# Performance work log

Hardware: AMD Instinct MI355X
Metric: run time of the kernel (lower is better)

Reference implementation:

```python
import jax, jax.numpy as jnp
import numpy as np

B, T = 32, 256
CHAR_V, BICHAR_V, CTYPE_V = 10000, 200000, 8
CD, BD, TD = 100, 100, 20
LIN, H = 200, 200
IN_DIMS = 2 * CD + 2 * BD + TD  # 420


def lstm_scan(xs, Wih, Whh, b, reverse=False):
    # xs: [T, B, LIN]; Wih: [4H, LIN]; Whh: [4H, H]; b: [4H]
    h0 = jnp.zeros((xs.shape[1], Whh.shape[1]), xs.dtype)
    c0 = jnp.zeros_like(h0)

    def step(carry, x):
        h, c = carry
        g = x @ Wih.T + h @ Whh.T + b  # [B, 4H]
        i, f, gg, o = jnp.split(g, 4, axis=-1)  # torch LSTMCell gate order
        c = jax.nn.sigmoid(f) * c + jax.nn.sigmoid(i) * jnp.tanh(gg)
        h = jax.nn.sigmoid(o) * jnp.tanh(c)
        return (h, c), h

    _, hs = jax.lax.scan(step, (h0, c0), xs, reverse=reverse)
    return hs  # [T, B, H]


def setup_inputs() -> dict:
    key = jax.random.key(0)
    ks = jax.random.split(key, 20)
    d = {
        "chars": jax.random.randint(ks[0], (B, T), 0, CHAR_V, jnp.int32),
        "left_bichar": jax.random.randint(ks[1], (B, T), 0, BICHAR_V, jnp.int32),
        "right_bichar": jax.random.randint(ks[2], (B, T), 0, BICHAR_V, jnp.int32),
        "extchars": jax.random.randint(ks[3], (B, T), 0, CHAR_V, jnp.int32),
        "extleft_bichar": jax.random.randint(ks[4], (B, T), 0, BICHAR_V, jnp.int32),
        "extright_bichar": jax.random.randint(ks[5], (B, T), 0, BICHAR_V, jnp.int32),
        "char_type": jax.random.randint(ks[6], (B, T), 0, CTYPE_V, jnp.int32),
        "E_char": jax.random.normal(ks[7], (CHAR_V, CD), jnp.float32) * 0.1,
        "E_extchar": jax.random.normal(ks[8], (CHAR_V, CD), jnp.float32) * 0.1,
        "E_bichar": jax.random.normal(ks[9], (BICHAR_V, BD), jnp.float32) * 0.1,
        "E_extbichar": jax.random.normal(ks[10], (BICHAR_V, BD), jnp.float32) * 0.1,
        "E_ctype": jax.random.normal(ks[11], (CTYPE_V, TD), jnp.float32) * 0.1,
        "fc_w": jax.random.normal(ks[12], (LIN, IN_DIMS), jnp.float32) * (1.0 / np.sqrt(IN_DIMS)),
        "fc_b": jnp.zeros((LIN,), jnp.float32),
        "Wih_l": jax.random.normal(ks[13], (4 * H, LIN), jnp.float32) * (1.0 / np.sqrt(LIN)),
        "Whh_l": jax.random.normal(ks[14], (4 * H, H), jnp.float32) * (1.0 / np.sqrt(H)),
        "b_l": jnp.zeros((4 * H,), jnp.float32),
        "Wih_r": jax.random.normal(ks[15], (4 * H, LIN), jnp.float32) * (1.0 / np.sqrt(LIN)),
        "Whh_r": jax.random.normal(ks[16], (4 * H, H), jnp.float32) * (1.0 / np.sqrt(H)),
        "b_r": jnp.zeros((4 * H,), jnp.float32),
    }
    return d


def reference(chars, left_bichar, right_bichar, extchars, extleft_bichar,
              extright_bichar, char_type, E_char, E_extchar, E_bichar,
              E_extbichar, E_ctype, fc_w, fc_b, Wih_l, Whh_l, b_l,
              Wih_r, Whh_r, b_r):
    c_e = E_char[chars]            # [B,T,CD]
    ec_e = E_extchar[extchars]
    lb_e = E_bichar[left_bichar]   # [B,T,BD]
    elb_e = E_extbichar[extleft_bichar]
    rb_e = E_bichar[right_bichar]
    erb_e = E_extbichar[extright_bichar]
    ct_e = E_ctype[char_type]      # [B,T,TD]

    left_total = jnp.concatenate([c_e, ec_e, lb_e, elb_e, ct_e], axis=2)
    right_total = jnp.concatenate([c_e, ec_e, rb_e, erb_e, ct_e], axis=2)

    left_x = jnp.tanh(left_total @ fc_w.T + fc_b).transpose(1, 0, 2)   # [T,B,LIN]
    right_x = jnp.tanh(right_total @ fc_w.T + fc_b).transpose(1, 0, 2)

    left_hs = lstm_scan(left_x, Wih_l, Whh_l, b_l, reverse=False)   # [T,B,H]
    right_hs = lstm_scan(right_x, Wih_r, Whh_r, b_r, reverse=True)  # [T,B,H]

    out = jnp.concatenate([left_hs, right_hs], axis=2).transpose(1, 0, 2)  # [B,T,2H]
    return out
```

## Files before the change

kernel.cpp:

```cpp
#include <hip/hip_runtime.h>
#include <stdint.h>

#define B_    32
#define T_    256
#define CD    100
#define BD    100
#define TD    20
#define LIN   200
#define HD    200
#define INDIM 420
#define G4    800

typedef __attribute__((ext_vector_type(8))) short bfrag8;
typedef __attribute__((ext_vector_type(4))) float f32x4v;

static __device__ __forceinline__ unsigned short f2bf(float f) {
  unsigned u = __float_as_uint(f);
  u = u + 0x7fffu + ((u >> 16) & 1u);
  return (unsigned short)(u >> 16);
}
static __device__ __forceinline__ float bf2f(unsigned short s) {
  return __uint_as_float(((unsigned)s) << 16);
}
static __device__ __forceinline__ float sigm(float x) {
  return __builtin_amdgcn_rcpf(1.0f + __builtin_amdgcn_exp2f(x * -1.4426950408889634f));
}
static __device__ __forceinline__ float tanhx(float x) {
  return 1.0f - 2.0f * __builtin_amdgcn_rcpf(1.0f + __builtin_amdgcn_exp2f(x * 2.8853900817779268f));
}

static __device__ __forceinline__ void mk_hilo(float4 a, float4 b, bfrag8& hi, bfrag8& lo) {
  float q[8] = {a.x, a.y, a.z, a.w, b.x, b.y, b.z, b.w};
  #pragma unroll
  for (int j = 0; j < 8; ++j) {
    unsigned short h = f2bf(q[j]);
    hi[j] = (short)h;
    lo[j] = (short)f2bf(q[j] - bf2f(h));
  }
}
static __device__ __forceinline__ bfrag8 mk_hi(float4 a, float4 b) {
  bfrag8 r;
  float q[8] = {a.x, a.y, a.z, a.w, b.x, b.y, b.z, b.w};
  #pragma unroll
  for (int j = 0; j < 8; ++j) r[j] = (short)f2bf(q[j]);
  return r;
}

__global__ void presplit_kernel(const float* __restrict__ fc_w,
                                const float* __restrict__ Wih_l,
                                const float* __restrict__ Wih_r,
                                unsigned short* __restrict__ fcw_hi,
                                unsigned short* __restrict__ fcw_lo,
                                unsigned short* __restrict__ wih_hi,
                                unsigned short* __restrict__ wih_lo) {
  int tid = blockIdx.x * blockDim.x + threadIdx.x;
  int stride = gridDim.x * blockDim.x;
  for (int i = tid; i < 13 * 14 * 512; i += stride) {
    int j = i & 7, l = (i >> 3) & 63, f = i >> 9;
    int kt = f % 14, nt = f / 14;
    int n = nt * 16 + (l & 15);
    int k = kt * 32 + ((l >> 4) << 3) + j;
    float v = (n < LIN && k < INDIM) ? fc_w[n * INDIM + k] : 0.0f;
    unsigned short h = f2bf(v);
    fcw_hi[i] = h;
    fcw_lo[i] = f2bf(v - bf2f(h));
  }
  for (int d = 0; d < 2; ++d) {
    const float* W = d ? Wih_r : Wih_l;
    unsigned short* oh = wih_hi + (size_t)d * 179200;
    unsigned short* ol = wih_lo + (size_t)d * 179200;
    for (int i = tid; i < 50 * 7 * 512; i += stride) {
      int j = i & 7, l = (i >> 3) & 63, f = i >> 9;
      int kt = f % 7, nt = f / 7;
      int np = nt * 16 + (l & 15);
      int no = (np & 3) * 200 + (np >> 2);
      int k = kt * 32 + ((l >> 4) << 3) + j;
      float v = (k < LIN) ? W[no * LIN + k] : 0.0f;
      unsigned short h = f2bf(v);
      oh[i] = h;
      ol[i] = f2bf(v - bf2f(h));
    }
  }
}

__global__ __launch_bounds__(256) void fc_kernel(
    const int* __restrict__ chars, const int* __restrict__ left_bichar,
    const int* __restrict__ right_bichar, const int* __restrict__ extchars,
    const int* __restrict__ extleft, const int* __restrict__ extright,
    const int* __restrict__ ctype,
    const float* __restrict__ E_char, const float* __restrict__ E_extchar,
    const float* __restrict__ E_bichar, const float* __restrict__ E_extbichar,
    const float* __restrict__ E_ctype, const float* __restrict__ fc_b,
    const unsigned short* __restrict__ fcw_hi, const unsigned short* __restrict__ fcw_lo,
    float* __restrict__ x) {
  __shared__ __align__(16) float feat[32 * 452];
  int rb = blockIdx.x;
  int dir = rb >> 8;
  int t = rb & 255;
  int tid = threadIdx.x;
  const int* bi  = dir ? right_bichar : left_bichar;
  const int* ebi = dir ? extright : extleft;

  for (int cc = tid; cc < 32 * 113; cc += 256) {
    int lr = cc / 113, kc = cc - lr * 113;
    int k = kc << 2;
    float4 v = make_float4(0.f, 0.f, 0.f, 0.f);
    if (k < INDIM) {
      int id; const float* tab; int kk; int wdt;
      if (k < 100)      { id = chars[lr * T_ + t];    tab = E_char;      kk = k;       wdt = 100; }
      else if (k < 200) { id = extchars[lr * T_ + t]; tab = E_extchar;   kk = k - 100; wdt = 100; }
      else if (k < 300) { id = bi[lr * T_ + t];       tab = E_bichar;    kk = k - 200; wdt = 100; }
      else if (k < 400) { id = ebi[lr * T_ + t];      tab = E_extbichar; kk = k - 300; wdt = 100; }
      else              { id = ctype[lr * T_ + t];    tab = E_ctype;     kk = k - 400; wdt = 20;  }
      v = *reinterpret_cast<const float4*>(tab + (size_t)id * wdt + kk);
    }
    *reinterpret_cast<float4*>(&feat[lr * 452 + k]) = v;
  }
  __syncthreads();

  int w = tid >> 6, l = tid & 63;
  int lrow = l & 15, lk8 = (l >> 4) << 3;
  f32x4v acc[8];
  #pragma unroll
  for (int i = 0; i < 8; ++i) acc[i] = (f32x4v){0.f, 0.f, 0.f, 0.f};

  for (int kt = 0; kt < 14; ++kt) {
    bfrag8 ah[2], al[2];
    #pragma unroll
    for (int mt = 0; mt < 2; ++mt) {
      const float* fp = &feat[(mt * 16 + lrow) * 452 + kt * 32 + lk8];
      float4 v0 = *reinterpret_cast<const float4*>(fp);
      float4 v1 = *reinterpret_cast<const float4*>(fp + 4);
      mk_hilo(v0, v1, ah[mt], al[mt]);
    }
    #pragma unroll
    for (int s = 0; s < 4; ++s) {
      int nt = w + (s << 2);
      if (nt < 13) {
        size_t fo = ((size_t)(nt * 14 + kt) * 64 + l) * 8;
        bfrag8 bh = *reinterpret_cast<const bfrag8*>(fcw_hi + fo);
        bfrag8 bl = *reinterpret_cast<const bfrag8*>(fcw_lo + fo);
        #pragma unroll
        for (int mt = 0; mt < 2; ++mt) {
          acc[s * 2 + mt] = __builtin_amdgcn_mfma_f32_16x16x32_bf16(ah[mt], bh, acc[s * 2 + mt], 0, 0, 0);
          acc[s * 2 + mt] = __builtin_amdgcn_mfma_f32_16x16x32_bf16(al[mt], bh, acc[s * 2 + mt], 0, 0, 0);
          acc[s * 2 + mt] = __builtin_amdgcn_mfma_f32_16x16x32_bf16(ah[mt], bl, acc[s * 2 + mt], 0, 0, 0);
        }
      }
    }
  }
  int r0 = rb * 32;
  #pragma unroll
  for (int s = 0; s < 4; ++s) {
    int nt = w + (s << 2);
    if (nt < 13) {
      int n = nt * 16 + lrow;
      if (n < LIN) {
        float bias = fc_b[n];
        #pragma unroll
        for (int mt = 0; mt < 2; ++mt) {
          #pragma unroll
          for (int rr = 0; rr < 4; ++rr) {
            int row = mt * 16 + ((l >> 4) << 2) + rr;
            x[(size_t)(r0 + row) * LIN + n] = tanhx(acc[s * 2 + mt][rr] + bias);
          }
        }
      }
    }
  }
}

__global__ __launch_bounds__(512) void xwih_kernel(
    const float* __restrict__ x, const unsigned short* __restrict__ wih_hi,
    const unsigned short* __restrict__ wih_lo, const float* __restrict__ b_l,
    const float* __restrict__ b_r, float* __restrict__ pre) {
  int bid = blockIdx.x;
  int dir = (bid >= 320) ? 1 : 0;
  int rem = bid - dir * 320;
  int rbm = rem / 5, nb = rem - rbm * 5;
  int m0 = rbm * 128, n0 = nb * 160;
  int tid = threadIdx.x, w = tid >> 6, l = tid & 63;
  int lrow = l & 15, lk8 = (l >> 4) << 3;
  const float* xd = x + (size_t)dir * 8192 * LIN;
  const unsigned short* wh = wih_hi + (size_t)dir * 179200;
  const unsigned short* wl = wih_lo + (size_t)dir * 179200;
  const float* bias = dir ? b_r : b_l;

  f32x4v acc[10];
  #pragma unroll
  for (int i = 0; i < 10; ++i) acc[i] = (f32x4v){0.f, 0.f, 0.f, 0.f};

  int row = m0 + w * 16 + lrow;
  for (int kt = 0; kt < 7; ++kt) {
    int kb = kt * 32 + lk8;
    bfrag8 ah = {0,0,0,0,0,0,0,0}, al = {0,0,0,0,0,0,0,0};
    if (kb <= 192) {
      const float* fp = xd + (size_t)row * LIN + kb;
      float4 v0 = *reinterpret_cast<const float4*>(fp);
      float4 v1 = *reinterpret_cast<const float4*>(fp + 4);
      mk_hilo(v0, v1, ah, al);
    }
    #pragma unroll
    for (int nt = 0; nt < 10; ++nt) {
      int ntg = nb * 10 + nt;
      size_t fo = ((size_t)(ntg * 7 + kt) * 64 + l) * 8;
      bfrag8 bh = *reinterpret_cast<const bfrag8*>(wh + fo);
      bfrag8 bl = *reinterpret_cast<const bfrag8*>(wl + fo);
      acc[nt] = __builtin_amdgcn_mfma_f32_16x16x32_bf16(ah, bh, acc[nt], 0, 0, 0);
      acc[nt] = __builtin_amdgcn_mfma_f32_16x16x32_bf16(al, bh, acc[nt], 0, 0, 0);
      acc[nt] = __builtin_amdgcn_mfma_f32_16x16x32_bf16(ah, bl, acc[nt], 0, 0, 0);
    }
  }
  #pragma unroll
  for (int nt = 0; nt < 10; ++nt) {
    int n = n0 + nt * 16 + lrow;
    float bb = bias[(n & 3) * 200 + (n >> 2)];
    int hcol = n >> 2, g = n & 3;
    int i6 = hcol >> 5;
    int hc5 = hcol & 31;
    int wv = hc5 >> 2, lhi = hc5 & 3;
    int chunk = (i6 < 6) ? (i6 * 8 + wv) : (48 + wv);
    #pragma unroll
    for (int rr = 0; rr < 4; ++rr) {
      int r2 = m0 + w * 16 + ((l >> 4) << 2) + rr;
      int t = r2 >> 5, b32 = r2 & 31;
      int hf2 = b32 >> 4, b = b32 & 15;
      int lane = b + 16 * lhi;
      size_t dst = ((((size_t)(dir * 2 + hf2) * 256 + t) * 50 + chunk) * 64 + lane) * 4 + g;
      pre[dst] = acc[nt][rr] + bb;
    }
  }
}

__global__ __launch_bounds__(512, 2) void lstm_kernel(
    const float* __restrict__ pre, const float* __restrict__ Whh_l,
    const float* __restrict__ Whh_r, float* __restrict__ out) {
  __shared__ __align__(16) unsigned short hbufA[3584];
  __shared__ __align__(16) unsigned short hbufB[3584];
  __shared__ __align__(16) unsigned short whx[35840];

  int bi = blockIdx.x;
  int dir = bi >> 1, half = bi & 1;
  const float* Whh = dir ? Whh_r : Whh_l;
  int tid = threadIdx.x, w = tid >> 6, l = tid & 63;
  int lrow = l & 15, lk8 = (l >> 4) << 3;

  bfrag8 Breg[5][7];
  #pragma unroll
  for (int i = 0; i < 5; ++i) {
    int np = (w + 8 * i) * 16 + lrow;
    int no = (np & 3) * 200 + (np >> 2);
    #pragma unroll
    for (int kt = 0; kt < 7; ++kt) {
      int kb = kt * 32 + lk8;
      bfrag8 bb = {0,0,0,0,0,0,0,0};
      if (kb <= 192) {
        const float* fp = Whh + (size_t)no * HD + kb;
        bb = mk_hi(*reinterpret_cast<const float4*>(fp),
                   *reinterpret_cast<const float4*>(fp + 4));
      }
      Breg[i][kt] = bb;
    }
  }
  for (int e = tid; e < 4480; e += 512) {
    int l2 = e & 63, f = e >> 6;
    int kt = f % 7, tile = f / 7;
    int np = (40 + tile) * 16 + (l2 & 15);
    int no = (np & 3) * 200 + (np >> 2);
    int kb = kt * 32 + ((l2 >> 4) << 3);
    bfrag8 bb = {0,0,0,0,0,0,0,0};
    if (kb <= 192) {
      const float* fp = Whh + (size_t)no * HD + kb;
      bb = mk_hi(*reinterpret_cast<const float4*>(fp),
                 *reinterpret_cast<const float4*>(fp + 4));
    }
    *reinterpret_cast<bfrag8*>(&whx[(size_t)e * 8]) = bb;
  }
  for (int e = tid; e < 896; e += 512) {
    reinterpret_cast<uint64_t*>(hbufA)[e] = 0;
    reinterpret_cast<uint64_t*>(hbufB)[e] = 0;
  }
  float c[7];
  #pragma unroll
  for (int i = 0; i < 7; ++i) c[i] = 0.f;

  int hbase = 4 * w + (l >> 4);
  int hw = (lrow + 16 * ((hbase >> 3) & 3)) * 8 + (hbase & 7);

  const float* psrcL = pre + ((size_t)(dir * 2 + half) * 256 + (dir ? 255 : 0)) * 12800
                     + w * 256 + (l << 2);
  const int pstep = dir ? -12800 : 12800;
  float* outp = out + (size_t)((half * 16 + lrow) * 256 + (dir ? 255 : 0)) * 400
              + dir * 200 + (l >> 4) + 4 * w;
  const int ostep = dir ? -400 : 400;

  __syncthreads();

  float4 pA[7], pB[7];
  #pragma unroll
  for (int i = 0; i < 6; ++i) pA[i] = *reinterpret_cast<const float4*>(psrcL + i * 2048);
  if (w < 2) pA[6] = *reinterpret_cast<const float4*>(psrcL + 12288);
  psrcL += pstep;

  auto STEP = [&](const unsigned short* rbuf, unsigned short* wbuf,
                  float4 (&pc)[7], float4 (&pn)[7]) {
    #pragma unroll
    for (int i = 0; i < 6; ++i) pn[i] = *reinterpret_cast<const float4*>(psrcL + i * 2048);
    if (w < 2) pn[6] = *reinterpret_cast<const float4*>(psrcL + 12288);
    psrcL += pstep;
    f32x4v acc[7];
    #pragma unroll
    for (int i = 0; i < 7; ++i) acc[i] = (f32x4v){0.f, 0.f, 0.f, 0.f};
    #pragma unroll
    for (int kt = 0; kt < 7; ++kt) {
      bfrag8 hf = *reinterpret_cast<const bfrag8*>(&rbuf[kt * 512 + l * 8]);
      #pragma unroll
      for (int i = 0; i < 5; ++i)
        acc[i] = __builtin_amdgcn_mfma_f32_16x16x32_bf16(Breg[i][kt], hf, acc[i], 0, 0, 0);
      bfrag8 b5 = *reinterpret_cast<const bfrag8*>(&whx[(w * 7 + kt) * 512 + l * 8]);
      acc[5] = __builtin_amdgcn_mfma_f32_16x16x32_bf16(b5, hf, acc[5], 0, 0, 0);
      if (w < 2) {
        bfrag8 b6 = *reinterpret_cast<const bfrag8*>(&whx[((8 + w) * 7 + kt) * 512 + l * 8]);
        acc[6] = __builtin_amdgcn_mfma_f32_16x16x32_bf16(b6, hf, acc[6], 0, 0, 0);
      }
    }
    #pragma unroll
    for (int i = 0; i < 7; ++i) {
      if (i < 6 || w < 2) {
        float ig = acc[i][0] + pc[i].x;
        float fg = acc[i][1] + pc[i].y;
        float gg = acc[i][2] + pc[i].z;
        float og = acc[i][3] + pc[i].w;
        float cv = sigm(fg) * c[i] + sigm(ig) * tanhx(gg);
        c[i] = cv;
        float h = sigm(og) * tanhx(cv);
        outp[32 * i] = h;
        wbuf[hw + i * 512] = f2bf(h);
      }
    }
    outp += ostep;
    __builtin_amdgcn_sched_barrier(0x1 | 0x2 | 0x4 | 0x8);
    asm volatile("s_waitcnt lgkmcnt(0)");
    __builtin_amdgcn_s_barrier();
    __builtin_amdgcn_sched_barrier(0x1 | 0x2 | 0x4 | 0x8);
  };

  for (int it = 0; it < 128; ++it) {
    STEP(hbufA, hbufB, pA, pB);
    STEP(hbufB, hbufA, pB, pA);
  }
}

extern "C" void kernel_launch(void* const* d_in, const int* in_sizes, int n_in,
                              void* d_out, int out_size, void* d_ws, size_t ws_size,
                              hipStream_t stream) {
  (void)in_sizes; (void)n_in; (void)out_size; (void)ws_size;
  const int* chars        = (const int*)d_in[0];
  const int* left_bichar  = (const int*)d_in[1];
  const int* right_bichar = (const int*)d_in[2];
  const int* extchars     = (const int*)d_in[3];
  const int* extleft      = (const int*)d_in[4];
  const int* extright     = (const int*)d_in[5];
  const int* ctype        = (const int*)d_in[6];
  const float* E_char      = (const float*)d_in[7];
  const float* E_extchar   = (const float*)d_in[8];
  const float* E_bichar    = (const float*)d_in[9];
  const float* E_extbichar = (const float*)d_in[10];
  const float* E_ctype     = (const float*)d_in[11];
  const float* fc_w  = (const float*)d_in[12];
  const float* fc_b  = (const float*)d_in[13];
  const float* Wih_l = (const float*)d_in[14];
  const float* Whh_l = (const float*)d_in[15];
  const float* b_l   = (const float*)d_in[16];
  const float* Wih_r = (const float*)d_in[17];
  const float* Whh_r = (const float*)d_in[18];
  const float* b_r   = (const float*)d_in[19];
  float* out = (float*)d_out;
  char* ws = (char*)d_ws;

  float* x   = (float*)(ws);
  float* pre = (float*)(ws + 13107200);
  unsigned short* fcw_hi = (unsigned short*)(ws + 65536000);
  unsigned short* fcw_lo = (unsigned short*)(ws + 65722368);
  unsigned short* wih_hi = (unsigned short*)(ws + 65908736);
  unsigned short* wih_lo = (unsigned short*)(ws + 66625536);

  presplit_kernel<<<256, 256, 0, stream>>>(fc_w, Wih_l, Wih_r, fcw_hi, fcw_lo, wih_hi, wih_lo);
  fc_kernel<<<512, 256, 0, stream>>>(chars, left_bichar, right_bichar, extchars,
                                     extleft, extright, ctype, E_char, E_extchar,
                                     E_bichar, E_extbichar, E_ctype, fc_b,
                                     fcw_hi, fcw_lo, x);
  xwih_kernel<<<640, 512, 0, stream>>>(x, wih_hi, wih_lo, b_l, b_r, pre);
  lstm_kernel<<<4, 512, 0, stream>>>(pre, Whh_l, Whh_r, out);
}
```

Before: 761.5 us.

## Keep more Whh tiles in registers, seed MFMA accumulators, fuse gate reciprocals

Moves one more 16-row Whh tile per wave from LDS into registers (Breg 5→6), so only waves 0-1 read the extra tile from LDS and the per-step LDS traffic for B fragments shrinks. The precomputed input gates now initialize the MFMA accumulators instead of being added afterwards. The gate nonlinearities are algebraically combined so the cell update needs one reciprocal instead of several, with exponent arguments clamped to avoid overflow. This raises register pressure under launch_bounds(512,2), which may cause spills, and it changes rounding slightly.

Result: faster. 738.4 us (-3.0%).

```diff
diff --git a/kernel.cpp b/kernel.cpp
--- a/kernel.cpp
+++ b/kernel.cpp
@@ -27,6 +27,9 @@
 }
 static __device__ __forceinline__ float tanhx(float x) {
   return 1.0f - 2.0f * __builtin_amdgcn_rcpf(1.0f + __builtin_amdgcn_exp2f(x * 2.8853900817779268f));
+}
+static __device__ __forceinline__ float clamp40(float x) {
+  return fminf(fmaxf(x, -40.0f), 40.0f);
 }
 
 static __device__ __forceinline__ void mk_hilo(float4 a, float4 b, bfrag8& hi, bfrag8& lo) {
@@ -237,7 +240,7 @@
     const float* __restrict__ Whh_r, float* __restrict__ out) {
   __shared__ __align__(16) unsigned short hbufA[3584];
   __shared__ __align__(16) unsigned short hbufB[3584];
-  __shared__ __align__(16) unsigned short whx[35840];
+  __shared__ __align__(16) unsigned short whx[7168];
 
   int bi = blockIdx.x;
   int dir = bi >> 1, half = bi & 1;
@@ -245,9 +248,9 @@
   int tid = threadIdx.x, w = tid >> 6, l = tid & 63;
   int lrow = l & 15, lk8 = (l >> 4) << 3;
 
-  bfrag8 Breg[5][7];
-  #pragma unroll
-  for (int i = 0; i < 5; ++i) {
+  bfrag8 Breg[6][7];
+  #pragma unroll
+  for (int i = 0; i < 6; ++i) {
     int np = (w + 8 * i) * 16 + lrow;
     int no = (np & 3) * 200 + (np >> 2);
     #pragma unroll
@@ -262,10 +265,10 @@
       Breg[i][kt] = bb;
     }
   }
-  for (int e = tid; e < 4480; e += 512) {
+  for (int e = tid; e < 896; e += 512) {
     int l2 = e & 63, f = e >> 6;
     int kt = f % 7, tile = f / 7;
-    int np = (40 + tile) * 16 + (l2 & 15);
+    int np = (48 + tile) * 16 + (l2 & 15);
     int no = (np & 3) * 200 + (np >> 2);
     int kb = kt * 32 + ((l2 >> 4) << 3);
     bfrag8 bb = {0,0,0,0,0,0,0,0};
@@ -298,9 +301,17 @@
 
   float4 pA[7], pB[7];
   #pragma unroll
+  for (int i = 0; i < 7; ++i) {
+    pA[i] = make_float4(0.f, 0.f, 0.f, 0.f);
+    pB[i] = make_float4(0.f, 0.f, 0.f, 0.f);
+  }
+  #pragma unroll
   for (int i = 0; i < 6; ++i) pA[i] = *reinterpret_cast<const float4*>(psrcL + i * 2048);
   if (w < 2) pA[6] = *reinterpret_cast<const float4*>(psrcL + 12288);
   psrcL += pstep;
+
+  const float NL  = -1.4426950408889634f;
+  const float N2L = -2.8853900817779268f;
 
   auto STEP = [&](const unsigned short* rbuf, unsigned short* wbuf,
                   float4 (&pc)[7], float4 (&pn)[7]) {
@@ -310,30 +321,37 @@
     psrcL += pstep;
     f32x4v acc[7];
     #pragma unroll
-    for (int i = 0; i < 7; ++i) acc[i] = (f32x4v){0.f, 0.f, 0.f, 0.f};
+    for (int i = 0; i < 7; ++i)
+      acc[i] = (f32x4v){pc[i].x, pc[i].y, pc[i].z, pc[i].w};
     #pragma unroll
     for (int kt = 0; kt < 7; ++kt) {
       bfrag8 hf = *reinterpret_cast<const bfrag8*>(&rbuf[kt * 512 + l * 8]);
       #pragma unroll
-      for (int i = 0; i < 5; ++i)
+      for (int i = 0; i < 6; ++i)
         acc[i] = __builtin_amdgcn_mfma_f32_16x16x32_bf16(Breg[i][kt], hf, acc[i], 0, 0, 0);
-      bfrag8 b5 = *reinterpret_cast<const bfrag8*>(&whx[(w * 7 + kt) * 512 + l * 8]);
-      acc[5] = __builtin_amdgcn_mfma_f32_16x16x32_bf16(b5, hf, acc[5], 0, 0, 0);
       if (w < 2) {
-        bfrag8 b6 = *reinterpret_cast<const bfrag8*>(&whx[((8 + w) * 7 + kt) * 512 + l * 8]);
+        bfrag8 b6 = *reinterpret_cast<const bfrag8*>(&whx[(w * 7 + kt) * 512 + l * 8]);
         acc[6] = __builtin_amdgcn_mfma_f32_16x16x32_bf16(b6, hf, acc[6], 0, 0, 0);
       }
     }
     #pragma unroll
     for (int i = 0; i < 7; ++i) {
       if (i < 6 || w < 2) {
-        float ig = acc[i][0] + pc[i].x;
-        float fg = acc[i][1] + pc[i].y;
-        float gg = acc[i][2] + pc[i].z;
-        float og = acc[i][3] + pc[i].w;
-        float cv = sigm(fg) * c[i] + sigm(ig) * tanhx(gg);
-        c[i] = cv;
-        float h = sigm(og) * tanhx(cv);
+        float ig = acc[i][0];
+        float fg = acc[i][1];
+        float gg = acc[i][2];
+        float og = acc[i][3];
+        float u  = __builtin_amdgcn_exp2f(clamp40(fg * NL));
+        float v  = __builtin_amdgcn_exp2f(clamp40(ig * NL));
+        float Wt = __builtin_amdgcn_exp2f(clamp40(gg * N2L));
+        float y  = __builtin_amdgcn_exp2f(clamp40(og * NL));
+        float pu = 1.f + u, pv = 1.f + v, pw = 1.f + Wt, py = 1.f + y;
+        float P  = pv * pw;
+        float r1 = __builtin_amdgcn_rcpf(pu * P);
+        float cn = (c[i] * P + pu * (1.f - Wt)) * r1;
+        c[i] = cn;
+        float Z  = __builtin_amdgcn_exp2f(clamp40(cn * N2L));
+        float h  = (1.f - Z) * __builtin_amdgcn_rcpf(py * (1.f + Z));
         outp[32 * i] = h;
         wbuf[hw + i * 512] = f2bf(h);
       }
```
